# Performance work log

Measured on AMD Instinct MI355X. Metric: run time of the kernel, lower is better.

Reference implementation:

```python
import jax, jax.numpy as jnp
import numpy as np

B, C, H, W = 2, 128, 192, 192
NH, WS, D = 4, 8, 2
HD = C // NH          # head dim = 32
N = WS * WS           # tokens per window = 64
SHIFT = WS // 2
HID = 4 * C
EPS = 1e-5
NWIN = (H // WS) * (W // WS)
SCALE = HD ** -0.5


def _rel_index():
    coords = np.stack(np.meshgrid(np.arange(WS), np.arange(WS), indexing='ij')).reshape(2, -1)
    rel = (coords[:, :, None] - coords[:, None, :]).transpose(1, 2, 0)
    rel[:, :, 0] += WS - 1
    rel[:, :, 1] += WS - 1
    rel[:, :, 0] *= 2 * WS - 1
    return jnp.asarray(rel.sum(-1))  # [N, N] int

REL_IDX = _rel_index()


def _attn_mask():
    # static shifted-window mask, exactly as BasicLayer.calculate_mask (pad = 0 here)
    img = np.zeros((H, W))
    cnt = 0
    sl = (slice(0, -WS), slice(-WS, -SHIFT), slice(-SHIFT, None))
    for hs in sl:
        for ws_ in sl:
            img[hs, ws_] = cnt
            cnt += 1
    mw = img.reshape(H // WS, WS, W // WS, WS).transpose(0, 2, 1, 3).reshape(-1, N)
    diff = mw[:, None, :] - mw[:, :, None]
    return jnp.asarray(np.where(diff != 0, -100.0, 0.0).astype(np.float32))  # [nW, N, N]

ATTN_MASK = _attn_mask()


def _win_part(x):  # [B,H,W,C] -> [B*nW, N, C]
    x = x.reshape(-1, H // WS, WS, W // WS, WS, C).transpose(0, 1, 3, 2, 4, 5)
    return x.reshape(-1, N, C)


def _win_rev(w):  # [B*nW, N, C] -> [B,H,W,C]
    x = w.reshape(-1, H // WS, W // WS, WS, WS, C).transpose(0, 1, 3, 2, 4, 5)
    return x.reshape(-1, H, W, C)


def _ln(x, g, b):
    m = jnp.mean(x, axis=-1, keepdims=True)
    v = jnp.mean((x - m) ** 2, axis=-1, keepdims=True)
    return (x - m) * jax.lax.rsqrt(v + EPS) * g + b


def _block(x, feat, shift, p):
    # x, feat: [B,H,W,C]
    shortcut = x
    if shift > 0:
        x = jnp.roll(x, (-shift, -shift), (1, 2))
        feat = jnp.roll(feat, (-shift, -shift), (1, 2))
    xw = _win_part(x)      # [B_, N, C]
    fw = _win_part(feat)
    q = (xw @ p['qW'] + p['qb']).reshape(-1, N, NH, HD).transpose(0, 2, 1, 3) * SCALE
    kv = (fw @ p['kvW'] + p['kvb']).reshape(-1, N, 2, NH, HD).transpose(2, 0, 3, 1, 4)
    k, v = kv[0], kv[1]
    attn = jnp.einsum('bhnd,bhmd->bhnm', q, k)  # [B_, NH, N, N]
    bias = p['relb'][REL_IDX].transpose(2, 0, 1)  # [NH, N, N]
    attn = attn + bias[None]
    if shift > 0:
        attn = attn.reshape(B, NWIN, NH, N, N) + ATTN_MASK[None, :, None]
        attn = attn.reshape(-1, NH, N, N)
    attn = jax.nn.softmax(attn, axis=-1)
    out = jnp.einsum('bhnm,bhmd->bhnd', attn, v).transpose(0, 2, 1, 3).reshape(-1, N, C)
    out = out @ p['pW'] + p['pb']
    x = _win_rev(out)  # [B,H,W,C]
    if shift > 0:
        x = jnp.roll(x, (shift, shift), (1, 2))
    x = shortcut + _ln(x @ p['mW'], p['n1g'], p['n1b'])
    h = jax.nn.gelu(x @ p['f1W'] + p['f1b'], approximate=False)
    x = x + _ln(h @ p['f2W'] + p['f2b'], p['n2g'], p['n2b'])
    return x


def _forward(x, source, target, qW, qb, kvW, kvb, pW, pb, relb, mW,
             n1g, n1b, f1W, f1b, f2W, f2b, n2g, n2b, convW, convb, pa):
    src_h = source.transpose(0, 2, 3, 1)  # BHWC
    tgt_h = target.transpose(0, 2, 3, 1)
    for d in range(D):
        shift = 0 if d % 2 == 0 else SHIFT
        p = dict(qW=qW[d], qb=qb[d], kvW=kvW[d], kvb=kvb[d], pW=pW[d], pb=pb[d],
                 relb=relb[d], mW=mW[d], n1g=n1g[d], n1b=n1b[d],
                 f1W=f1W[d], f1b=f1b[d], f2W=f2W[d], f2b=f2b[d],
                 n2g=n2g[d], n2b=n2b[d])
        xh = x.transpose(0, 2, 3, 1)
        sa = _block(xh, src_h, shift, p)
        ta = _block(xh, tgt_h, shift, p)
        cat = jnp.concatenate([sa, ta], axis=-1).transpose(0, 3, 1, 2)  # [B,2C,H,W]
        y = jax.lax.conv_general_dilated(
            cat, convW[d], window_strides=(1, 1), padding=((1, 1), (1, 1)),
            dimension_numbers=('NCHW', 'OIHW', 'NCHW')) + convb[d][None, :, None, None]
        a = pa[d][None, :, None, None]
        x = jnp.where(y >= 0, y, a * y)  # PReLU
    return x


def setup_inputs() -> dict:
    key = jax.random.key(0)
    ks = jax.random.split(key, 24)
    r = lambda i, shape, s=0.02: jax.random.normal(ks[i], shape, jnp.float32) * s
    return dict(
        x=jax.random.normal(ks[0], (B, C, H, W), jnp.float32),
        source=jax.random.normal(ks[1], (B, C, H, W), jnp.float32),
        target=jax.random.normal(ks[2], (B, C, H, W), jnp.float32),
        qW=r(3, (D, C, C)), qb=r(4, (D, C)),
        kvW=r(5, (D, C, 2 * C)), kvb=r(6, (D, 2 * C)),
        pW=r(7, (D, C, C)), pb=r(8, (D, C)),
        relb=r(9, (D, (2 * WS - 1) ** 2, NH)),
        mW=r(10, (D, C, C)),
        n1g=jnp.ones((D, C), jnp.float32), n1b=jnp.zeros((D, C), jnp.float32),
        f1W=r(11, (D, C, HID)), f1b=r(12, (D, HID)),
        f2W=r(13, (D, HID, C)), f2b=r(14, (D, C)),
        n2g=jnp.ones((D, C), jnp.float32), n2b=jnp.zeros((D, C), jnp.float32),
        convW=r(15, (D, C, 2 * C, 3, 3), 0.05), convb=r(16, (D, C)),
        pa=jnp.full((D, C), 0.25, jnp.float32),
    )


def reference(x, source, target, qW, qb, kvW, kvb, pW, pb, relb, mW,
              n1g, n1b, f1W, f1b, f2W, f2b, n2g, n2b, convW, convb, pa):
    return _forward(x, source, target, qW, qb, kvW, kvb, pW, pb, relb, mW,
                    n1g, n1b, f1W, f1b, f2W, f2b, n2g, n2b, convW, convb, pa)
```

## Files before the change

### kernel.cpp

```cpp
#include <hip/hip_runtime.h>
#include <math.h>

#define SCALEf 0.1767766952966369f

typedef short s16x8 __attribute__((ext_vector_type(8)));
typedef float f32x4 __attribute__((ext_vector_type(4)));
typedef unsigned u32x4 __attribute__((ext_vector_type(4)));

__device__ __forceinline__ short f2bf(float f) {
    unsigned u = __float_as_uint(f);
    u += 0x7FFF + ((u >> 16) & 1);
    return (short)(u >> 16);
}
__device__ __forceinline__ float gelu_f(float u) {
    float z = 1.5957691216057308f * u * (1.0f + 0.044715f * u * u);
    return u / (1.0f + __expf(-z));
}
__device__ __forceinline__ s16x8 ld8bf(const float* p) {
    float4 u0 = *(const float4*)p;
    float4 u1 = *(const float4*)(p + 4);
    s16x8 a;
    a[0] = f2bf(u0.x); a[1] = f2bf(u0.y); a[2] = f2bf(u0.z); a[3] = f2bf(u0.w);
    a[4] = f2bf(u1.x); a[5] = f2bf(u1.y); a[6] = f2bf(u1.z); a[7] = f2bf(u1.w);
    return a;
}
__device__ __forceinline__ s16x8 u4_to_s8(unsigned a0, unsigned a1, unsigned a2, unsigned a3) {
    union { u32x4 a; s16x8 b; } c;
    c.a[0] = a0; c.a[1] = a1; c.a[2] = a2; c.a[3] = a3;
    return c.b;
}
__device__ __forceinline__ int region_code(int h, int w) {
    return ((h < 184) ? 0 : (h < 188 ? 3 : 6)) + ((w < 184) ? 0 : (w < 188 ? 1 : 2));
}

__global__ __launch_bounds__(256) void k_transpose(
    const float* __restrict__ x, const float* __restrict__ s, const float* __restrict__ t,
    float* __restrict__ xo, short* __restrict__ xb, short* __restrict__ sb, short* __restrict__ tb)
{
    int which = blockIdx.z;
    const float* in = which == 0 ? x : (which == 1 ? s : t);
    short* outb = which == 0 ? xb : (which == 1 ? sb : tb);
    __shared__ float tile[32][33];
    int by = blockIdx.y;
    int b = by >> 2;
    int c0 = (by & 3) * 32;
    int p0 = blockIdx.x * 32;
    int tx = threadIdx.x & 31;
    int ty = threadIdx.x >> 5;
    const float* ip = in + (size_t)b * 128 * 36864;
    #pragma unroll
    for (int k = 0; k < 4; ++k) {
        int c = c0 + ty + 8 * k;
        tile[ty + 8 * k][tx] = ip[(size_t)c * 36864 + p0 + tx];
    }
    __syncthreads();
    #pragma unroll
    for (int k = 0; k < 4; ++k) {
        int p = p0 + ty + 8 * k;
        float v = tile[tx][ty + 8 * k];
        size_t off = (size_t)b * 36864 * 128 + (size_t)p * 128 + c0 + tx;
        if (which == 0) xo[off] = v;
        outb[off] = f2bf(v);
    }
}

__global__ __launch_bounds__(256) void k_fold_proj(
    const float* __restrict__ pW, const float* __restrict__ pb,
    const float* __restrict__ mW, short* __restrict__ W2T, float* __restrict__ b2)
{
    if (blockIdx.x < 64) {
        int o = blockIdx.x * 256 + threadIdx.x;
        int i = o >> 7, c = o & 127;
        float acc = 0.f;
        for (int k = 0; k < 128; ++k) acc = fmaf(pW[i * 128 + k], mW[k * 128 + c], acc);
        W2T[c * 128 + i] = f2bf(acc);
    } else {
        int c = threadIdx.x;
        if (c < 128) {
            float acc = 0.f;
            for (int k = 0; k < 128; ++k) acc = fmaf(pb[k], mW[k * 128 + c], acc);
            b2[c] = acc;
        }
    }
}

__global__ __launch_bounds__(256) void k_prep(
    const float* __restrict__ f1W, const float* __restrict__ f2W,
    const float* __restrict__ convW, const float* __restrict__ qW,
    const float* __restrict__ kvW,
    short* __restrict__ W1T, short* __restrict__ W2Tm, short* __restrict__ cwb,
    short* __restrict__ qWT, short* __restrict__ kvWT)
{
    int idx = blockIdx.x * 256 + threadIdx.x;
    if (idx < 65536) {
        int n = idx >> 7, k = idx & 127;
        W1T[idx] = f2bf(f1W[k * 512 + n]);
    } else if (idx < 131072) {
        int j = idx - 65536;
        int n = j >> 9, k = j & 511;
        W2Tm[j] = f2bf(f2W[k * 128 + n]);
    } else if (idx < 425984) {
        int j = idx - 131072;
        int ci = j & 255;
        int co = (j >> 8) & 127;
        int k9 = j >> 15;
        cwb[j] = f2bf(convW[(co * 256 + ci) * 9 + k9]);
    } else if (idx < 442368) {
        int j = idx - 425984;
        int n = j >> 7, k = j & 127;
        qWT[j] = f2bf(qW[k * 128 + n]);
    } else if (idx < 475136) {
        int j = idx - 442368;
        int n = j >> 7, k = j & 127;
        kvWT[j] = f2bf(kvW[k * 256 + n]);
    }
}

__global__ __launch_bounds__(256, 3) void k_attn_mfma(
    const float* __restrict__ xh, const short* __restrict__ xbf,
    const short* __restrict__ sbf, const short* __restrict__ tbf,
    const short* __restrict__ qWT, const float* __restrict__ qb,
    const short* __restrict__ kvWT, const float* __restrict__ kvb,
    const float* __restrict__ relb, const short* __restrict__ W2T, const float* __restrict__ b2,
    const float* __restrict__ g1, const float* __restrict__ b1,
    float* __restrict__ sa, float* __restrict__ ta, int shift)
{
    __shared__ short s_q[64 * 136];
    __shared__ short s_kk[64 * 136];
    __shared__ short s_vt[128 * 72];

    int gid = blockIdx.x;
    int branch = gid >= 1152;
    int wid = branch ? gid - 1152 : gid;
    const short* featb = branch ? tbf : sbf;
    float* outb = branch ? ta : sa;
    int b = wid / 576;
    int wi = wid - b * 576;
    int wh = wi / 24, ww = wi - wh * 24;

    int tid = threadIdx.x;
    int h = tid >> 6;
    int lane = tid & 63;
    int ln = lane & 15, quad = lane >> 4;
    int ho = h * 32;
    int koff = quad * 8;

    size_t rowoff[4];
    #pragma unroll
    for (int mt = 0; mt < 4; ++mt) {
        int tok = mt * 16 + ln;
        int ti = tok >> 3, tj = tok & 7;
        int hh = wh * 8 + ti + shift; if (hh >= 192) hh -= 192;
        int wz = ww * 8 + tj + shift; if (wz >= 192) wz -= 192;
        rowoff[mt] = (((size_t)b * 192 + hh) * 192 + wz) * 128;
    }

    {
        f32x4 acc[4][2] = {};
        for (int kc = 0; kc < 4; ++kc) {
            s16x8 a[4];
            #pragma unroll
            for (int mt = 0; mt < 4; ++mt) a[mt] = *(const s16x8*)(xbf + rowoff[mt] + kc * 32 + koff);
            #pragma unroll
            for (int nt = 0; nt < 2; ++nt) {
                s16x8 bfr = *(const s16x8*)(qWT + (ho + nt * 16 + ln) * 128 + kc * 32 + koff);
                #pragma unroll
                for (int mt = 0; mt < 4; ++mt)
                    acc[mt][nt] = __builtin_amdgcn_mfma_f32_16x16x32_bf16(a[mt], bfr, acc[mt][nt], 0, 0, 0);
            }
        }
        #pragma unroll
        for (int nt = 0; nt < 2; ++nt) {
            int col = ho + nt * 16 + ln;
            float bb = qb[col];
            #pragma unroll
            for (int mt = 0; mt < 4; ++mt)
                #pragma unroll
                for (int r = 0; r < 4; ++r)
                    s_q[(mt * 16 + quad * 4 + r) * 136 + col] = f2bf((acc[mt][nt][r] + bb) * SCALEf);
        }
    }

    {
        f32x4 acc[4][2] = {};
        for (int kc = 0; kc < 4; ++kc) {
            s16x8 a[4];
            #pragma unroll
            for (int mt = 0; mt < 4; ++mt) a[mt] = *(const s16x8*)(featb + rowoff[mt] + kc * 32 + koff);
            #pragma unroll
            for (int nt = 0; nt < 2; ++nt) {
                s16x8 bfr = *(const s16x8*)(kvWT + (ho + nt * 16 + ln) * 128 + kc * 32 + koff);
                #pragma unroll
                for (int mt = 0; mt < 4; ++mt)
                    acc[mt][nt] = __builtin_amdgcn_mfma_f32_16x16x32_bf16(a[mt], bfr, acc[mt][nt], 0, 0, 0);
            }
        }
        #pragma unroll
        for (int nt = 0; nt < 2; ++nt) {
            int col = ho + nt * 16 + ln;
            float bb = kvb[col];
            #pragma unroll
            for (int mt = 0; mt < 4; ++mt)
                #pragma unroll
                for (int r = 0; r < 4; ++r)
                    s_kk[(mt * 16 + quad * 4 + r) * 136 + col] = f2bf(acc[mt][nt][r] + bb);
        }
    }

    {
        f32x4 acc[2][4] = {};
        for (int kc = 0; kc < 4; ++kc) {
            s16x8 aw[2];
            #pragma unroll
            for (int md = 0; md < 2; ++md)
                aw[md] = *(const s16x8*)(kvWT + (128 + ho + md * 16 + ln) * 128 + kc * 32 + koff);
            #pragma unroll
            for (int nt = 0; nt < 4; ++nt) {
                s16x8 bfr = *(const s16x8*)(featb + rowoff[nt] + kc * 32 + koff);
                #pragma unroll
                for (int md = 0; md < 2; ++md)
                    acc[md][nt] = __builtin_amdgcn_mfma_f32_16x16x32_bf16(aw[md], bfr, acc[md][nt], 0, 0, 0);
            }
        }
        #pragma unroll
        for (int md = 0; md < 2; ++md)
            #pragma unroll
            for (int r = 0; r < 4; ++r) {
                int d = ho + md * 16 + quad * 4 + r;
                float bb = kvb[128 + d];
                #pragma unroll
                for (int nt = 0; nt < 4; ++nt)
                    s_vt[d * 72 + nt * 16 + ln] = f2bf(acc[md][nt][r] + bb);
            }
    }

    int cq_code[4];
    int ckp[4];
    if (shift) {
        #pragma unroll
        for (int nq = 0; nq < 4; ++nq) {
            int q = nq * 16 + ln;
            cq_code[nq] = region_code(wh * 8 + (q >> 3), ww * 8 + (q & 7));
        }
        #pragma unroll
        for (int mtk = 0; mtk < 4; ++mtk) {
            int c = 0;
            #pragma unroll
            for (int r = 0; r < 4; ++r) {
                int kt = mtk * 16 + quad * 4 + r;
                c |= region_code(wh * 8 + (kt >> 3), ww * 8 + (kt & 7)) << (8 * r);
            }
            ckp[mtk] = c;
        }
    }

    f32x4 acco[4][2] = {};
    #pragma unroll
    for (int nq = 0; nq < 4; ++nq) {
        s16x8 bq = *(const s16x8*)(s_q + (nq * 16 + ln) * 136 + ho + koff);
        f32x4 st[4];
        #pragma unroll
        for (int mtk = 0; mtk < 4; ++mtk) {
            s16x8 aK = *(const s16x8*)(s_kk + (mtk * 16 + ln) * 136 + ho + koff);
            f32x4 z = {};
            st[mtk] = __builtin_amdgcn_mfma_f32_16x16x32_bf16(aK, bq, z, 0, 0, 0);
        }
        int q = nq * 16 + ln;
        int qti = q >> 3, qtj = q & 7;
        float vals[16];
        #pragma unroll
        for (int mtk = 0; mtk < 4; ++mtk)
            #pragma unroll
            for (int r = 0; r < 4; ++r) {
                int kt = mtk * 16 + quad * 4 + r;
                int dr = qti - (kt >> 3) + 7, dc = qtj - (kt & 7) + 7;
                float v = st[mtk][r] + relb[(dr * 15 + dc) * 4 + h];
                if (shift && cq_code[nq] != ((ckp[mtk] >> (8 * r)) & 255)) v -= 100.0f;
                vals[mtk * 4 + r] = v;
            }
        float mx = vals[0];
        #pragma unroll
        for (int i = 1; i < 16; ++i) mx = fmaxf(mx, vals[i]);
        mx = fmaxf(mx, __shfl_xor(mx, 16));
        mx = fmaxf(mx, __shfl_xor(mx, 32));
        float sum = 0.f;
        #pragma unroll
        for (int i = 0; i < 16; ++i) { vals[i] = __expf(vals[i] - mx); sum += vals[i]; }
        sum += __shfl_xor(sum, 16);
        sum += __shfl_xor(sum, 32);
        float inv = 1.0f / sum;
        unsigned pd[4][2];
        #pragma unroll
        for (int mtk = 0; mtk < 4; ++mtk)
            #pragma unroll
            for (int rp = 0; rp < 2; ++rp) {
                unsigned lo16 = (unsigned short)f2bf(vals[mtk * 4 + 2 * rp] * inv);
                unsigned hi16 = (unsigned short)f2bf(vals[mtk * 4 + 2 * rp + 1] * inv);
                pd[mtk][rp] = lo16 | (hi16 << 16);
            }
        #pragma unroll
        for (int kc2 = 0; kc2 < 2; ++kc2) {
            unsigned ad[4];
            #pragma unroll
            for (int rp = 0; rp < 2; ++rp) {
                unsigned X0 = pd[2 * kc2][rp], X1 = pd[2 * kc2 + 1][rp];
                unsigned B0 = __shfl_xor(X0, 16);
                unsigned C0 = __shfl_xor(X0, 32);
                unsigned D0 = __shfl_xor(B0, 32);
                unsigned B1 = __shfl_xor(X1, 16);
                unsigned C1 = __shfl_xor(X1, 32);
                unsigned D1 = __shfl_xor(B1, 32);
                unsigned lo = quad == 0 ? X0 : quad == 1 ? D0 : quad == 2 ? C1 : B1;
                unsigned hi = quad == 0 ? B0 : quad == 1 ? C0 : quad == 2 ? D1 : X1;
                ad[rp] = lo; ad[2 + rp] = hi;
            }
            s16x8 ap = u4_to_s8(ad[0], ad[1], ad[2], ad[3]);
            #pragma unroll
            for (int nt2 = 0; nt2 < 2; ++nt2) {
                s16x8 bv = *(const s16x8*)(s_vt + (ho + nt2 * 16 + ln) * 72 + kc2 * 32 + koff);
                acco[nq][nt2] = __builtin_amdgcn_mfma_f32_16x16x32_bf16(ap, bv, acco[nq][nt2], 0, 0, 0);
            }
        }
    }
    #pragma unroll
    for (int nq = 0; nq < 4; ++nq)
        #pragma unroll
        for (int nt2 = 0; nt2 < 2; ++nt2)
            #pragma unroll
            for (int r = 0; r < 4; ++r)
                s_q[(nq * 16 + quad * 4 + r) * 136 + ho + nt2 * 16 + ln] = f2bf(acco[nq][nt2][r]);
    __syncthreads();

    {
        f32x4 accp[8] = {};
        for (int kc = 0; kc < 4; ++kc) {
            s16x8 a = *(const s16x8*)(s_q + (h * 16 + ln) * 136 + kc * 32 + koff);
            #pragma unroll
            for (int nt = 0; nt < 8; ++nt) {
                s16x8 bfr = *(const s16x8*)(W2T + (nt * 16 + ln) * 128 + kc * 32 + koff);
                accp[nt] = __builtin_amdgcn_mfma_f32_16x16x32_bf16(a, bfr, accp[nt], 0, 0, 0);
            }
        }
        #pragma unroll
        for (int nt = 0; nt < 8; ++nt) {
            float bb = b2[nt * 16 + ln];
            #pragma unroll
            for (int r = 0; r < 4; ++r) accp[nt][r] += bb;
        }
        #pragma unroll
        for (int r = 0; r < 4; ++r) {
            float sm = 0.f, sq = 0.f;
            #pragma unroll
            for (int nt = 0; nt < 8; ++nt) { float v = accp[nt][r]; sm += v; sq = fmaf(v, v, sq); }
            sm += __shfl_xor(sm, 1); sq += __shfl_xor(sq, 1);
            sm += __shfl_xor(sm, 2); sq += __shfl_xor(sq, 2);
            sm += __shfl_xor(sm, 4); sq += __shfl_xor(sq, 4);
            sm += __shfl_xor(sm, 8); sq += __shfl_xor(sq, 8);
            float mean = sm * (1.0f / 128.0f);
            float var = sq * (1.0f / 128.0f) - mean * mean;
            float rstd = rsqrtf(var + 1e-5f);
            int token = h * 16 + quad * 4 + r;
            int ti = token >> 3, tj = token & 7;
            int hh = wh * 8 + ti + shift; if (hh >= 192) hh -= 192;
            int wz = ww * 8 + tj + shift; if (wz >= 192) wz -= 192;
            size_t rb = (((size_t)b * 192 + hh) * 192 + wz) * 128;
            #pragma unroll
            for (int nt = 0; nt < 8; ++nt) {
                int col = nt * 16 + ln;
                float o = xh[rb + col] + fmaf((accp[nt][r] - mean) * rstd, g1[col], b1[col]);
                outb[rb + col] = o;
            }
        }
    }
}

__global__ __launch_bounds__(256, 3) void k_mlp_mfma(
    const float* __restrict__ sab, const float* __restrict__ tab,
    const short* __restrict__ W1T, const float* __restrict__ f1b,
    const short* __restrict__ W2T, const float* __restrict__ f2b,
    const float* __restrict__ g2, const float* __restrict__ b2n,
    short* __restrict__ catb)
{
    int gid = blockIdx.x;
    int br = gid >= 576;
    int bi = br ? gid - 576 : gid;
    const float* X = br ? tab : sab;

    int tid = threadIdx.x;
    int w = tid >> 6, lane = tid & 63;
    int ln = lane & 15, quad = lane >> 4;
    int koff = quad * 8;
    int tok0 = bi * 128 + w * 32;

    s16x8 xf[2][4];
    #pragma unroll
    for (int tt = 0; tt < 2; ++tt)
        #pragma unroll
        for (int kc = 0; kc < 4; ++kc)
            xf[tt][kc] = ld8bf(X + (size_t)(tok0 + tt * 16 + ln) * 128 + kc * 32 + koff);

    f32x4 acc2[2][8] = {};

    for (int ch = 0; ch < 16; ++ch) {
        f32x4 acc1[2][2] = {};
        #pragma unroll
        for (int kc = 0; kc < 4; ++kc) {
            s16x8 aw[2];
            #pragma unroll
            for (int nh = 0; nh < 2; ++nh)
                aw[nh] = *(const s16x8*)(W1T + (size_t)(ch * 32 + nh * 16 + ln) * 128 + kc * 32 + koff);
            #pragma unroll
            for (int nh = 0; nh < 2; ++nh)
                #pragma unroll
                for (int tt = 0; tt < 2; ++tt)
                    acc1[nh][tt] = __builtin_amdgcn_mfma_f32_16x16x32_bf16(aw[nh], xf[tt][kc], acc1[nh][tt], 0, 0, 0);
        }
        float4 fb0 = *(const float4*)(f1b + ch * 32 + quad * 4);
        float4 fb1 = *(const float4*)(f1b + ch * 32 + 16 + quad * 4);
        #pragma unroll
        for (int tt = 0; tt < 2; ++tt) {
            unsigned pd0[2], pd1[2];
            {
                float h0 = gelu_f(acc1[0][tt][0] + fb0.x);
                float h1 = gelu_f(acc1[0][tt][1] + fb0.y);
                float h2 = gelu_f(acc1[0][tt][2] + fb0.z);
                float h3 = gelu_f(acc1[0][tt][3] + fb0.w);
                pd0[0] = (unsigned short)f2bf(h0) | ((unsigned)(unsigned short)f2bf(h1) << 16);
                pd0[1] = (unsigned short)f2bf(h2) | ((unsigned)(unsigned short)f2bf(h3) << 16);
                float g0 = gelu_f(acc1[1][tt][0] + fb1.x);
                float g1v = gelu_f(acc1[1][tt][1] + fb1.y);
                float g2v = gelu_f(acc1[1][tt][2] + fb1.z);
                float g3 = gelu_f(acc1[1][tt][3] + fb1.w);
                pd1[0] = (unsigned short)f2bf(g0) | ((unsigned)(unsigned short)f2bf(g1v) << 16);
                pd1[1] = (unsigned short)f2bf(g2v) | ((unsigned)(unsigned short)f2bf(g3) << 16);
            }
            unsigned ad[4];
            #pragma unroll
            for (int rp = 0; rp < 2; ++rp) {
                unsigned X0 = pd0[rp], X1 = pd1[rp];
                unsigned B0 = __shfl_xor(X0, 16);
                unsigned C0 = __shfl_xor(X0, 32);
                unsigned D0 = __shfl_xor(B0, 32);
                unsigned B1 = __shfl_xor(X1, 16);
                unsigned C1 = __shfl_xor(X1, 32);
                unsigned D1 = __shfl_xor(B1, 32);
                unsigned lo = quad == 0 ? X0 : quad == 1 ? D0 : quad == 2 ? C1 : B1;
                unsigned hi = quad == 0 ? B0 : quad == 1 ? C0 : quad == 2 ? D1 : X1;
                ad[rp] = lo; ad[2 + rp] = hi;
            }
            s16x8 bh = u4_to_s8(ad[0], ad[1], ad[2], ad[3]);
            #pragma unroll
            for (int nt = 0; nt < 8; ++nt) {
                s16x8 aw2 = *(const s16x8*)(W2T + (size_t)(nt * 16 + ln) * 512 + ch * 32 + koff);
                acc2[tt][nt] = __builtin_amdgcn_mfma_f32_16x16x32_bf16(aw2, bh, acc2[tt][nt], 0, 0, 0);
            }
        }
    }

    #pragma unroll
    for (int tt = 0; tt < 2; ++tt) {
        int tok = tok0 + tt * 16 + ln;
        float sm = 0.f, sq = 0.f;
        #pragma unroll
        for (int nt = 0; nt < 8; ++nt) {
            float4 fb2 = *(const float4*)(f2b + nt * 16 + quad * 4);
            acc2[tt][nt][0] += fb2.x; acc2[tt][nt][1] += fb2.y;
            acc2[tt][nt][2] += fb2.z; acc2[tt][nt][3] += fb2.w;
            #pragma unroll
            for (int r = 0; r < 4; ++r) {
                float v = acc2[tt][nt][r];
                sm += v; sq = fmaf(v, v, sq);
            }
        }
        sm += __shfl_xor(sm, 16); sq += __shfl_xor(sq, 16);
        sm += __shfl_xor(sm, 32); sq += __shfl_xor(sq, 32);
        float mean = sm * (1.0f / 128.0f);
        float var = sq * (1.0f / 128.0f) - mean * mean;
        float rstd = rsqrtf(var + 1e-5f);
        #pragma unroll
        for (int nt = 0; nt < 8; ++nt) {
            int c0 = nt * 16 + quad * 4;
            float4 xr = *(const float4*)(X + (size_t)tok * 128 + c0);
            float4 gg = *(const float4*)(g2 + c0);
            float4 bb = *(const float4*)(b2n + c0);
            unsigned short o0 = (unsigned short)f2bf(xr.x + fmaf((acc2[tt][nt][0] - mean) * rstd, gg.x, bb.x));
            unsigned short o1 = (unsigned short)f2bf(xr.y + fmaf((acc2[tt][nt][1] - mean) * rstd, gg.y, bb.y));
            unsigned short o2 = (unsigned short)f2bf(xr.z + fmaf((acc2[tt][nt][2] - mean) * rstd, gg.z, bb.z));
            unsigned short o3 = (unsigned short)f2bf(xr.w + fmaf((acc2[tt][nt][3] - mean) * rstd, gg.w, bb.w));
            uint2 st;
            st.x = (unsigned)o0 | ((unsigned)o1 << 16);
            st.y = (unsigned)o2 | ((unsigned)o3 << 16);
            *(uint2*)(catb + (size_t)tok * 256 + br * 128 + c0) = st;
        }
    }
}

__global__ __launch_bounds__(256) void k_conv_mfma(
    const short* __restrict__ catb, const short* __restrict__ cwb,
    const float* __restrict__ bias, const float* __restrict__ pa,
    float* __restrict__ out, short* __restrict__ obf, int nchw)
{
    __shared__ short s_in[136 * 264];
    int gid = blockIdx.x;
    int b = gid / 576;
    int r0 = gid - b * 576;
    int hp = r0 / 6;
    int wt = r0 - hp * 6;
    int h0 = hp * 2, w0 = wt * 32;
    int tid = threadIdx.x;

    for (int idx = tid; idx < 4352; idx += 256) {
        int row = idx >> 5, seg = idx & 31;
        int dh = row / 34, wc34 = row - dh * 34;
        int hh = h0 - 1 + dh;
        int wc = w0 - 1 + wc34;
        uint4 v = make_uint4(0u, 0u, 0u, 0u);
        if (hh >= 0 && hh < 192 && wc >= 0 && wc < 192)
            v = *(const uint4*)(catb + (((size_t)b * 192 + hh) * 192 + wc) * 256 + seg * 8);
        *(uint4*)(&s_in[row * 264 + seg * 8]) = v;
    }
    __syncthreads();

    int w = tid >> 6, lane = tid & 63;
    int ln = lane & 15, quad = lane >> 4;
    f32x4 acc[4][2] = {};

    #pragma unroll
    for (int kh = 0; kh < 3; ++kh) {
        #pragma unroll
        for (int kw = 0; kw < 3; ++kw) {
            const short* wbase = cwb + (size_t)((kh * 3 + kw) * 128 + w * 32) * 256;
            const short* ab[4];
            #pragma unroll
            for (int mt = 0; mt < 4; ++mt) {
                int prow = ((mt >> 1) + kh) * 34 + (mt & 1) * 16 + ln + kw;
                ab[mt] = s_in + prow * 264 + quad * 8;
            }
            for (int kc = 0; kc < 8; ++kc) {
                s16x8 bfr[2];
                #pragma unroll
                for (int nt = 0; nt < 2; ++nt)
                    bfr[nt] = *(const s16x8*)(wbase + (nt * 16 + ln) * 256 + kc * 32 + quad * 8);
                s16x8 afr[4];
                #pragma unroll
                for (int mt = 0; mt < 4; ++mt)
                    afr[mt] = *(const s16x8*)(ab[mt] + kc * 32);
                #pragma unroll
                for (int nt = 0; nt < 2; ++nt)
                    #pragma unroll
                    for (int mt = 0; mt < 4; ++mt)
                        acc[mt][nt] = __builtin_amdgcn_mfma_f32_16x16x32_bf16(afr[mt], bfr[nt], acc[mt][nt], 0, 0, 0);
            }
        }
    }

    if (!nchw) {
        #pragma unroll
        for (int nt = 0; nt < 2; ++nt) {
            int co = w * 32 + nt * 16 + ln;
            float bs = bias[co], pv = pa[co];
            #pragma unroll
            for (int mt = 0; mt < 4; ++mt) {
                int pr = mt >> 1;
                #pragma unroll
                for (int r = 0; r < 4; ++r) {
                    int pw = (mt & 1) * 16 + quad * 4 + r;
                    float v = acc[mt][nt][r] + bs;
                    v = (v >= 0.f) ? v : pv * v;
                    size_t off = (((size_t)b * 192 + h0 + pr) * 192 + w0 + pw) * 128 + co;
                    out[off] = v;
                    obf[off] = f2bf(v);
                }
            }
        }
    } else {
        __syncthreads();
        float* s_out = (float*)s_in;
        #pragma unroll
        for (int nt = 0; nt < 2; ++nt) {
            int co = w * 32 + nt * 16 + ln;
            float bs = bias[co], pv = pa[co];
            #pragma unroll
            for (int mt = 0; mt < 4; ++mt) {
                int pos0 = (mt >> 1) * 32 + (mt & 1) * 16 + quad * 4;
                #pragma unroll
                for (int r = 0; r < 4; ++r) {
                    float v = acc[mt][nt][r] + bs;
                    v = (v >= 0.f) ? v : pv * v;
                    s_out[co * 65 + pos0 + r] = v;
                }
            }
        }
        __syncthreads();
        for (int idx = tid; idx < 2048; idx += 256) {
            int co = idx >> 4;
            int pr = (idx >> 3) & 1;
            int sg = idx & 7;
            const float* sp = s_out + co * 65 + pr * 32 + sg * 4;
            float4 v = make_float4(sp[0], sp[1], sp[2], sp[3]);
            *(float4*)(out + (((size_t)b * 128 + co) * 192 + h0 + pr) * 192 + w0 + sg * 4) = v;
        }
    }
}

extern "C" void kernel_launch(void* const* d_in, const int* in_sizes, int n_in,
                              void* d_out, int out_size, void* d_ws, size_t ws_size,
                              hipStream_t stream)
{
    const float* x    = (const float*)d_in[0];
    const float* src  = (const float*)d_in[1];
    const float* tgt  = (const float*)d_in[2];
    const float* qW   = (const float*)d_in[3];
    const float* qb   = (const float*)d_in[4];
    const float* kvW  = (const float*)d_in[5];
    const float* kvb  = (const float*)d_in[6];
    const float* pW   = (const float*)d_in[7];
    const float* pb   = (const float*)d_in[8];
    const float* relb = (const float*)d_in[9];
    const float* mW   = (const float*)d_in[10];
    const float* n1g  = (const float*)d_in[11];
    const float* n1b  = (const float*)d_in[12];
    const float* f1W  = (const float*)d_in[13];
    const float* f1b  = (const float*)d_in[14];
    const float* f2W  = (const float*)d_in[15];
    const float* f2b  = (const float*)d_in[16];
    const float* n2g  = (const float*)d_in[17];
    const float* n2b  = (const float*)d_in[18];
    const float* convW= (const float*)d_in[19];
    const float* convb= (const float*)d_in[20];
    const float* pa   = (const float*)d_in[21];
    float* out = (float*)d_out;

    const size_t FR = (size_t)2 * 192 * 192 * 128;
    float* ws   = (float*)d_ws;
    float* xh   = ws;
    float* sab  = ws + FR;
    float* tab  = ws + 2 * FR;
    float* b2   = ws + 3 * FR;
    short* W1T  = (short*)(b2 + 128);
    short* W2Tm = W1T + 65536;
    short* cwb  = W2Tm + 65536;
    short* qWT  = cwb + 294912;
    short* kvWT = qWT + 16384;
    short* W2Tp = kvWT + 32768;
    short* xbf  = W2Tp + 16384;
    short* sbf  = xbf + FR;
    short* tbf  = sbf + FR;
    short* catb = (short*)sab;

    k_transpose<<<dim3(1152, 8, 3), 256, 0, stream>>>(x, src, tgt, xh, xbf, sbf, tbf);

    for (int d = 0; d < 2; ++d) {
        int shift = d ? 4 : 0;
        k_fold_proj<<<65, 256, 0, stream>>>(pW + d * 16384, pb + d * 128, mW + d * 16384, W2Tp, b2);
        k_prep<<<1856, 256, 0, stream>>>(f1W + d * 65536, f2W + d * 65536,
                                         convW + d * 294912, qW + d * 16384, kvW + d * 32768,
                                         W1T, W2Tm, cwb, qWT, kvWT);
        k_attn_mfma<<<2304, 256, 0, stream>>>(xh, xbf, sbf, tbf,
            qWT, qb + d * 128, kvWT, kvb + d * 256,
            relb + d * 900, W2Tp, b2, n1g + d * 128, n1b + d * 128, sab, tab, shift);
        k_mlp_mfma<<<1152, 256, 0, stream>>>(sab, tab, W1T, f1b + d * 512,
            W2Tm, f2b + d * 128, n2g + d * 128, n2b + d * 128, catb);
        k_conv_mfma<<<1152, 256, 0, stream>>>(catb, cwb, convb + d * 128, pa + d * 128,
            d == 1 ? out : xh, xbf, d == 1 ? 1 : 0);
    }
}
```

Baseline: 1.128 ms.

## Store attention outputs as bf16 and shrink MLP blocks to 16 tokens per wave

The attention kernel now writes its residual+LayerNorm output as bf16 instead of fp32, so the MLP kernel reads half the bytes and loads bf16 fragments directly with no conversion. The MLP kernel is changed to 128-thread blocks with 16 tokens per wave, launched over 4× as many blocks. It also hoists the W2 weight loads ahead of the first GEMM in each chunk. Workspace buffers are rearranged to hold separate bf16 intermediate arrays. The cost is extra rounding of the residual path to bf16 and more weight reloads per token, since each wave now reuses its weight fragments across fewer tokens.

```diff
diff --git a/kernel.cpp b/kernel.cpp
--- a/kernel.cpp
+++ b/kernel.cpp
@@ -12,17 +12,11 @@
     u += 0x7FFF + ((u >> 16) & 1);
     return (short)(u >> 16);
 }
+__device__ __forceinline__ float bf2f_lo(unsigned u) { return __uint_as_float(u << 16); }
+__device__ __forceinline__ float bf2f_hi(unsigned u) { return __uint_as_float(u & 0xffff0000u); }
 __device__ __forceinline__ float gelu_f(float u) {
     float z = 1.5957691216057308f * u * (1.0f + 0.044715f * u * u);
     return u / (1.0f + __expf(-z));
-}
-__device__ __forceinline__ s16x8 ld8bf(const float* p) {
-    float4 u0 = *(const float4*)p;
-    float4 u1 = *(const float4*)(p + 4);
-    s16x8 a;
-    a[0] = f2bf(u0.x); a[1] = f2bf(u0.y); a[2] = f2bf(u0.z); a[3] = f2bf(u0.w);
-    a[4] = f2bf(u1.x); a[5] = f2bf(u1.y); a[6] = f2bf(u1.z); a[7] = f2bf(u1.w);
-    return a;
 }
 __device__ __forceinline__ s16x8 u4_to_s8(unsigned a0, unsigned a1, unsigned a2, unsigned a3) {
     union { u32x4 a; s16x8 b; } c;
@@ -123,7 +117,7 @@
     const short* __restrict__ kvWT, const float* __restrict__ kvb,
     const float* __restrict__ relb, const short* __restrict__ W2T, const float* __restrict__ b2,
     const float* __restrict__ g1, const float* __restrict__ b1,
-    float* __restrict__ sa, float* __restrict__ ta, int shift)
+    short* __restrict__ sa, short* __restrict__ ta, int shift)
 {
     __shared__ short s_q[64 * 136];
     __shared__ short s_kk[64 * 136];
@@ -133,7 +127,7 @@
     int branch = gid >= 1152;
     int wid = branch ? gid - 1152 : gid;
     const short* featb = branch ? tbf : sbf;
-    float* outb = branch ? ta : sa;
+    short* outb = branch ? ta : sa;
     int b = wid / 576;
     int wi = wid - b * 576;
     int wh = wi / 24, ww = wi - wh * 24;
@@ -368,107 +362,99 @@
             for (int nt = 0; nt < 8; ++nt) {
                 int col = nt * 16 + ln;
                 float o = xh[rb + col] + fmaf((accp[nt][r] - mean) * rstd, g1[col], b1[col]);
-                outb[rb + col] = o;
-            }
-        }
-    }
-}
-
-__global__ __launch_bounds__(256, 3) void k_mlp_mfma(
-    const float* __restrict__ sab, const float* __restrict__ tab,
+                outb[rb + col] = f2bf(o);
+            }
+        }
+    }
+}
+
+__global__ __launch_bounds__(128, 4) void k_mlp_mfma(
+    const short* __restrict__ sab, const short* __restrict__ tab,
     const short* __restrict__ W1T, const float* __restrict__ f1b,
     const short* __restrict__ W2T, const float* __restrict__ f2b,
     const float* __restrict__ g2, const float* __restrict__ b2n,
     short* __restrict__ catb)
 {
     int gid = blockIdx.x;
-    int br = gid >= 576;
-    int bi = br ? gid - 576 : gid;
-    const float* X = br ? tab : sab;
+    int br = gid >= 2304;
+    int bi = br ? gid - 2304 : gid;
+    const short* X = br ? tab : sab;
 
     int tid = threadIdx.x;
     int w = tid >> 6, lane = tid & 63;
     int ln = lane & 15, quad = lane >> 4;
     int koff = quad * 8;
-    int tok0 = bi * 128 + w * 32;
-
-    s16x8 xf[2][4];
+    int tok0 = bi * 32 + w * 16;
+    int tok = tok0 + ln;
+
+    s16x8 xf[4];
     #pragma unroll
-    for (int tt = 0; tt < 2; ++tt)
-        #pragma unroll
-        for (int kc = 0; kc < 4; ++kc)
-            xf[tt][kc] = ld8bf(X + (size_t)(tok0 + tt * 16 + ln) * 128 + kc * 32 + koff);
-
-    f32x4 acc2[2][8] = {};
+    for (int kc = 0; kc < 4; ++kc)
+        xf[kc] = *(const s16x8*)(X + (size_t)tok * 128 + kc * 32 + koff);
+
+    f32x4 acc2[8] = {};
 
     for (int ch = 0; ch < 16; ++ch) {
-        f32x4 acc1[2][2] = {};
+        s16x8 aw2[8];
+        #pragma unroll
+        for (int nt = 0; nt < 8; ++nt)
+            aw2[nt] = *(const s16x8*)(W2T + (size_t)(nt * 16 + ln) * 512 + ch * 32 + koff);
+
+        f32x4 acc1[2] = {};
         #pragma unroll
         for (int kc = 0; kc < 4; ++kc) {
-            s16x8 aw[2];
-            #pragma unroll
-            for (int nh = 0; nh < 2; ++nh)
-                aw[nh] = *(const s16x8*)(W1T + (size_t)(ch * 32 + nh * 16 + ln) * 128 + kc * 32 + koff);
-            #pragma unroll
-            for (int nh = 0; nh < 2; ++nh)
-                #pragma unroll
-                for (int tt = 0; tt < 2; ++tt)
-                    acc1[nh][tt] = __builtin_amdgcn_mfma_f32_16x16x32_bf16(aw[nh], xf[tt][kc], acc1[nh][tt], 0, 0, 0);
+            s16x8 aw0 = *(const s16x8*)(W1T + (size_t)(ch * 32 + ln) * 128 + kc * 32 + koff);
+            s16x8 aw1 = *(const s16x8*)(W1T + (size_t)(ch * 32 + 16 + ln) * 128 + kc * 32 + koff);
+            acc1[0] = __builtin_amdgcn_mfma_f32_16x16x32_bf16(aw0, xf[kc], acc1[0], 0, 0, 0);
+            acc1[1] = __builtin_amdgcn_mfma_f32_16x16x32_bf16(aw1, xf[kc], acc1[1], 0, 0, 0);
         }
         float4 fb0 = *(const float4*)(f1b + ch * 32 + quad * 4);
         float4 fb1 = *(const float4*)(f1b + ch * 32 + 16 + quad * 4);
-        #pragma unroll
-        for (int tt = 0; tt < 2; ++tt) {
-            unsigned pd0[2], pd1[2];
-            {
-                float h0 = gelu_f(acc1[0][tt][0] + fb0.x);
-                float h1 = gelu_f(acc1[0][tt][1] + fb0.y);
-                float h2 = gelu_f(acc1[0][tt][2] + fb0.z);
-                float h3 = gelu_f(acc1[0][tt][3] + fb0.w);
-                pd0[0] = (unsigned short)f2bf(h0) | ((unsigned)(unsigned short)f2bf(h1) << 16);
-                pd0[1] = (unsigned short)f2bf(h2) | ((unsigned)(unsigned short)f2bf(h3) << 16);
-                float g0 = gelu_f(acc1[1][tt][0] + fb1.x);
-                float g1v = gelu_f(acc1[1][tt][1] + fb1.y);
-                float g2v = gelu_f(acc1[1][tt][2] + fb1.z);
-                float g3 = gelu_f(acc1[1][tt][3] + fb1.w);
-                pd1[0] = (unsigned short)f2bf(g0) | ((unsigned)(unsigned short)f2bf(g1v) << 16);
-                pd1[1] = (unsigned short)f2bf(g2v) | ((unsigned)(unsigned short)f2bf(g3) << 16);
-            }
-            unsigned ad[4];
-            #pragma unroll
-            for (int rp = 0; rp < 2; ++rp) {
-                unsigned X0 = pd0[rp], X1 = pd1[rp];
-                unsigned B0 = __shfl_xor(X0, 16);
-                unsigned C0 = __shfl_xor(X0, 32);
-                unsigned D0 = __shfl_xor(B0, 32);
-                unsigned B1 = __shfl_xor(X1, 16);
-                unsigned C1 = __shfl_xor(X1, 32);
-                unsigned D1 = __shfl_xor(B1, 32);
-                unsigned lo = quad == 0 ? X0 : quad == 1 ? D0 : quad == 2 ? C1 : B1;
-                unsigned hi = quad == 0 ? B0 : quad == 1 ? C0 : quad == 2 ? D1 : X1;
-                ad[rp] = lo; ad[2 + rp] = hi;
-            }
-            s16x8 bh = u4_to_s8(ad[0], ad[1], ad[2], ad[3]);
-            #pragma unroll
-            for (int nt = 0; nt < 8; ++nt) {
-                s16x8 aw2 = *(const s16x8*)(W2T + (size_t)(nt * 16 + ln) * 512 + ch * 32 + koff);
-                acc2[tt][nt] = __builtin_amdgcn_mfma_f32_16x16x32_bf16(aw2, bh, acc2[tt][nt], 0, 0, 0);
-            }
-        }
-    }
-
-    #pragma unroll
-    for (int tt = 0; tt < 2; ++tt) {
-        int tok = tok0 + tt * 16 + ln;
+        unsigned pd0[2], pd1[2];
+        {
+            float h0 = gelu_f(acc1[0][0] + fb0.x);
+            float h1 = gelu_f(acc1[0][1] + fb0.y);
+            float h2 = gelu_f(acc1[0][2] + fb0.z);
+            float h3 = gelu_f(acc1[0][3] + fb0.w);
+            pd0[0] = (unsigned short)f2bf(h0) | ((unsigned)(unsigned short)f2bf(h1) << 16);
+            pd0[1] = (unsigned short)f2bf(h2) | ((unsigned)(unsigned short)f2bf(h3) << 16);
+            float g0 = gelu_f(acc1[1][0] + fb1.x);
+            float g1v = gelu_f(acc1[1][1] + fb1.y);
+            float g2v = gelu_f(acc1[1][2] + fb1.z);
+            float g3 = gelu_f(acc1[1][3] + fb1.w);
+            pd1[0] = (unsigned short)f2bf(g0) | ((unsigned)(unsigned short)f2bf(g1v) << 16);
+            pd1[1] = (unsigned short)f2bf(g2v) | ((unsigned)(unsigned short)f2bf(g3) << 16);
+        }
+        unsigned ad[4];
+        #pragma unroll
+        for (int rp = 0; rp < 2; ++rp) {
+            unsigned X0 = pd0[rp], X1 = pd1[rp];
+            unsigned B0 = __shfl_xor(X0, 16);
+            unsigned C0 = __shfl_xor(X0, 32);
+            unsigned D0 = __shfl_xor(B0, 32);
+            unsigned B1 = __shfl_xor(X1, 16);
+            unsigned C1 = __shfl_xor(X1, 32);
+            unsigned D1 = __shfl_xor(B1, 32);
+            unsigned lo = quad == 0 ? X0 : quad == 1 ? D0 : quad == 2 ? C1 : B1;
+            unsigned hi = quad == 0 ? B0 : quad == 1 ? C0 : quad == 2 ? D1 : X1;
+            ad[rp] = lo; ad[2 + rp] = hi;
+        }
+        s16x8 bh = u4_to_s8(ad[0], ad[1], ad[2], ad[3]);
+        #pragma unroll
+        for (int nt = 0; nt < 8; ++nt)
+            acc2[nt] = __builtin_amdgcn_mfma_f32_16x16x32_bf16(aw2[nt], bh, acc2[nt], 0, 0, 0);
+    }
+
+    {
         float sm = 0.f, sq = 0.f;
         #pragma unroll
         for (int nt = 0; nt < 8; ++nt) {
             float4 fb2 = *(const float4*)(f2b + nt * 16 + quad * 4);
-            acc2[tt][nt][0] += fb2.x; acc2[tt][nt][1] += fb2.y;
-            acc2[tt][nt][2] += fb2.z; acc2[tt][nt][3] += fb2.w;
+            acc2[nt][0] += fb2.x; acc2[nt][1] += fb2.y;
+            acc2[nt][2] += fb2.z; acc2[nt][3] += fb2.w;
             #pragma unroll
             for (int r = 0; r < 4; ++r) {
-                float v = acc2[tt][nt][r];
+                float v = acc2[nt][r];
                 sm += v; sq = fmaf(v, v, sq);
             }
         }
@@ -480,13 +466,15 @@
         #pragma unroll
         for (int nt = 0; nt < 8; ++nt) {
             int c0 = nt * 16 + quad * 4;
-            float4 xr = *(const float4*)(X + (size_t)tok * 128 + c0);
+            uint2 xr2 = *(const uint2*)(X + (size_t)tok * 128 + c0);
             float4 gg = *(const float4*)(g2 + c0);
             float4 bb = *(const float4*)(b2n + c0);
-            unsigned short o0 = (unsigned short)f2bf(xr.x + fmaf((acc2[tt][nt][0] - mean) * rstd, gg.x, bb.x));
-            unsigned short o1 = (unsigned short)f2bf(xr.y + fmaf((acc2[tt][nt][1] - mean) * rstd, gg.y, bb.y));
-            unsigned short o2 = (unsigned short)f2bf(xr.z + fmaf((acc2[tt][nt][2] - mean) * rstd, gg.z, bb.z));
-            unsigned short o3 = (unsigned short)f2bf(xr.w + fmaf((acc2[tt][nt][3] - mean) * rstd, gg.w, bb.w));
+            float x0 = bf2f_lo(xr2.x), x1 = bf2f_hi(xr2.x);
+            float x2 = bf2f_lo(xr2.y), x3 = bf2f_hi(xr2.y);
+            unsigned short o0 = (unsigned short)f2bf(x0 + fmaf((acc2[nt][0] - mean) * rstd, gg.x, bb.x));
+            unsigned short o1 = (unsigned short)f2bf(x1 + fmaf((acc2[nt][1] - mean) * rstd, gg.y, bb.y));
+            unsigned short o2 = (unsigned short)f2bf(x2 + fmaf((acc2[nt][2] - mean) * rstd, gg.z, bb.z));
+            unsigned short o3 = (unsigned short)f2bf(x3 + fmaf((acc2[nt][3] - mean) * rstd, gg.w, bb.w));
             uint2 st;
             st.x = (unsigned)o0 | ((unsigned)o1 << 16);
             st.y = (unsigned)o2 | ((unsigned)o3 << 16);
@@ -634,9 +622,7 @@
     const size_t FR = (size_t)2 * 192 * 192 * 128;
     float* ws   = (float*)d_ws;
     float* xh   = ws;
-    float* sab  = ws + FR;
-    float* tab  = ws + 2 * FR;
-    float* b2   = ws + 3 * FR;
+    float* b2   = ws + FR;
     short* W1T  = (short*)(b2 + 128);
     short* W2Tm = W1T + 65536;
     short* cwb  = W2Tm + 65536;
@@ -646,7 +632,9 @@
     short* xbf  = W2Tp + 16384;
     short* sbf  = xbf + FR;
     short* tbf  = sbf + FR;
-    short* catb = (short*)sab;
+    short* sbb  = tbf + FR;
+    short* tbb  = sbb + FR;
+    short* catb = tbb + FR;
 
     k_transpose<<<dim3(1152, 8, 3), 256, 0, stream>>>(x, src, tgt, xh, xbf, sbf, tbf);
 
@@ -658,8 +646,8 @@
                                          W1T, W2Tm, cwb, qWT, kvWT);
         k_attn_mfma<<<2304, 256, 0, stream>>>(xh, xbf, sbf, tbf,
             qWT, qb + d * 128, kvWT, kvb + d * 256,
-            relb + d * 900, W2Tp, b2, n1g + d * 128, n1b + d * 128, sab, tab, shift);
-        k_mlp_mfma<<<1152, 256, 0, stream>>>(sab, tab, W1T, f1b + d * 512,
+            relb + d * 900, W2Tp, b2, n1g + d * 128, n1b + d * 128, sbb, tbb, shift);
+        k_mlp_mfma<<<4608, 128, 0, stream>>>(sbb, tbb, W1T, f1b + d * 512,
             W2Tm, f2b + d * 128, n2g + d * 128, n2b + d * 128, catb);
         k_conv_mfma<<<1152, 256, 0, stream>>>(catb, cwb, convb + d * 128, pa + d * 128,
             d == 1 ? out : xh, xbf, d == 1 ? 1 : 0);
```

New measurement: 1.383 ms. 1.23x slower.
